# Optimization experiments

Measured on AMD Instinct MI355X. Metric: run time of the kernel, lower is better.

## Reference

```python
import jax, jax.numpy as jnp
import numpy as np

B, H, S, D = 2, 16, 2048, 128

def setup_inputs() -> dict:
    key = jax.random.key(0)
    kq, kk, kv = jax.random.split(key, 3)
    Q = jax.random.normal(kq, (B, H, S, D), dtype=jnp.float32)
    K = jax.random.normal(kk, (B, H, S, D), dtype=jnp.float32)
    V = jax.random.normal(kv, (B, H, S, D), dtype=jnp.float32)
    mask = jnp.tril(jnp.ones((S, S), dtype=bool))  # causal: 1 = keep
    return {"Q": Q, "K": K, "V": V, "mask": mask}

def reference(Q, K, V, mask):
    d_k = Q.shape[-1]
    scale = 1.0 / jnp.sqrt(jnp.asarray(d_k, dtype=Q.dtype))
    # [B,H,S,S] scores, matching the naive materialized implementation's math
    scores = jnp.einsum('bhqd,bhkd->bhqk', Q, K) * scale
    scores = jnp.where(mask, scores, jnp.asarray(-1e9, dtype=scores.dtype))
    attn = jax.nn.softmax(scores, axis=-1)
    return jnp.einsum('bhqk,bhkd->bhqd', attn, V)
```

## Files before the change

kernel.cpp:

```cpp
#include <hip/hip_runtime.h>
#include <hip/hip_bf16.h>
#include <stdint.h>

typedef __attribute__((ext_vector_type(8)))  __bf16 bf16x8;
typedef __attribute__((ext_vector_type(16))) float  f32x16;

#define B_  2
#define H_  16
#define S_  2048
#define D_  128
#define BH_ (B_*H_)

__device__ __forceinline__ uint32_t f2bf1(float f){
  uint32_t u = __builtin_bit_cast(uint32_t, f);
  return (u + 0x7fffu + ((u >> 16) & 1u)) >> 16;
}
__device__ __forceinline__ uint32_t pk2(float a, float b){
  return f2bf1(a) | (f2bf1(b) << 16);
}
__device__ __forceinline__ float bf2f(unsigned short u){
  return __builtin_bit_cast(float, (uint32_t)u << 16);
}
__device__ __forceinline__ float max3f(float a, float b, float c){
  return fmaxf(fmaxf(a, b), c);
}
__device__ __forceinline__ float ex2(float x){
  float r;
  asm("v_exp_f32 %0, %1" : "=v"(r) : "v"(x));
  return r;
}

__device__ __forceinline__ void gld16(const void* g, void* l){
  __builtin_amdgcn_global_load_lds(
      (const __attribute__((address_space(1))) void*)g,
      (__attribute__((address_space(3))) void*)(uintptr_t)l, 16, 0, 0);
}

__device__ const unsigned char SPLIT_TAB[24] = {
  15*4+1,15*4+2, 7*4+0, 14*4+1,14*4+2, 13*4+1,13*4+2, 6*4+0,
  12*4+1,12*4+2, 11*4+1,11*4+2, 5*4+0, 10*4+1,10*4+2, 9*4+1,9*4+2,
  4*4+0, 8*4+1,8*4+2, 3*4+0, 2*4+0, 1*4+0, 0*4+0
};

__global__ void prep(const float* __restrict__ K, const float* __restrict__ V,
                     unsigned short* __restrict__ Kb, unsigned short* __restrict__ Vt){
  __shared__ __attribute__((aligned(16))) unsigned short t[64*68];
  const int kv0 = blockIdx.x * 64, d0 = blockIdx.y * 64, bh = blockIdx.z;
  const int tid = threadIdx.x;
  const float* Vp = V + (size_t)bh * S_ * D_;
  const float* Kp = K + (size_t)bh * S_ * D_;
  unsigned short* Ko = Kb + (size_t)bh * S_ * D_;
  for (int i = 0; i < 4; i++){
    int f = tid + i*256;
    int kv = f >> 4, c4 = f & 15;
    size_t idx = (size_t)(kv0+kv)*D_ + d0 + c4*4;
    float4 k = *(const float4*)(Kp + idx);
    *(uint2*)(Ko + idx) = make_uint2(pk2(k.x,k.y), pk2(k.z,k.w));
  }
  for (int i = 0; i < 4; i++){
    int f = tid + i*256;
    int kv = f >> 4, c4 = f & 15;
    float4 v = *(const float4*)(Vp + (size_t)(kv0+kv)*D_ + d0 + c4*4);
    *(uint2*)&t[kv*68 + c4*4] = make_uint2(pk2(v.x,v.y), pk2(v.z,v.w));
  }
  __syncthreads();
  unsigned short* Vo = Vt + (size_t)bh * D_ * S_;
  for (int i = 0; i < 4; i++){
    int g = tid + i*256;
    int d = g >> 4, c = g & 15, kv = c*4;
    ushort4 o;
    o.x = t[(kv+0)*68 + d];
    o.y = t[(kv+1)*68 + d];
    o.z = t[(kv+2)*68 + d];
    o.w = t[(kv+3)*68 + d];
    *(ushort4*)(Vo + (size_t)(d0+d)*S_ + kv0 + kv) = o;
  }
}

__global__ __launch_bounds__(256, 3)
void attn_fwd(const float* __restrict__ Q, const unsigned short* __restrict__ Kb,
              const unsigned short* __restrict__ Vt, float* __restrict__ Out,
              unsigned short* __restrict__ Opart, float* __restrict__ MLpart,
              int splitFlag){
  __shared__ __attribute__((aligned(16))) unsigned short Klds[2][32*128];
  __shared__ __attribute__((aligned(16))) unsigned short Vlds[2][128*32];

  const int bi = blockIdx.x;
  const int bh = (bi & 7) + 8*((bi >> 3) & 3);
  const int u  = bi >> 5;
  int qb, mode;
  if (splitFlag){ int c = SPLIT_TAB[u]; qb = c >> 2; mode = c & 3; }
  else { qb = (u < 8) ? (15 - u) : (u - 8); mode = 0; }

  const int tid  = threadIdx.x;
  const int wave = tid >> 6, lane = tid & 63;
  const int q32  = lane & 31, hf = lane >> 5;
  const int wq0  = qb*128 + wave*32;
  const int t0   = (mode == 2) ? 2*qb + 2 : 0;
  const int tEnd = (mode == 1) ? 2*qb + 2 : 4*qb + 4;
  const int dtw  = (mode == 1) ? (1 << 30) : (4*qb + wave);
  const float qs = 0.08838834764831845f * 1.44269504088896f;

  const char* Kg = (const char*)(Kb + (size_t)bh * S_ * D_);
  const char* Vg = (const char*)(Vt + (size_t)bh * D_ * S_);

  uint32_t koff[2], voff[2];
  #pragma unroll
  for (int i = 0; i < 2; i++){
    int kr = wave*8 + i*4 + (lane >> 4);
    koff[i] = kr*256 + (((lane & 15) ^ (kr & 15)) << 4);
    int vr = wave*32 + i*16 + (lane >> 2);
    voff[i] = vr*(S_*2) + (((lane & 3) ^ ((vr >> 1) & 3)) << 4);
  }

  auto stage = [&](int buf, int t){
    const char* kp = Kg + t*8192;
    const char* vp = Vg + t*64;
    char* kd = (char*)&Klds[buf][0] + wave*2048;
    char* vd = (char*)&Vlds[buf][0] + wave*2048;
    #pragma unroll
    for (int i = 0; i < 2; i++){
      gld16(kp + koff[i], kd + i*1024);
      gld16(vp + voff[i], vd + i*1024);
    }
  };

  uint4 qf[8];
  {
    const float* Qp = Q + ((size_t)bh * S_ + (wq0 + q32)) * D_ + hf*8;
    #pragma unroll
    for (int ds = 0; ds < 8; ds++){
      float4 a = *(const float4*)(Qp + ds*16);
      float4 b = *(const float4*)(Qp + ds*16 + 4);
      bf16x8 q8;
      q8[0] = (__bf16)(a.x*qs); q8[1] = (__bf16)(a.y*qs);
      q8[2] = (__bf16)(a.z*qs); q8[3] = (__bf16)(a.w*qs);
      q8[4] = (__bf16)(b.x*qs); q8[5] = (__bf16)(b.y*qs);
      q8[6] = (__bf16)(b.z*qs); q8[7] = (__bf16)(b.w*qs);
      qf[ds] = __builtin_bit_cast(uint4, q8);
    }
  }

  f32x16 o[4];
  #pragma unroll
  for (int db = 0; db < 4; db++) o[db] = (f32x16)(0.f);
  float m_run = -INFINITY, l_run = 0.f;

  stage(0, t0);
  __syncthreads();

  int cur = 0;
  for (int t = t0; t < tEnd; ++t){
    if (t + 1 < tEnd) stage(cur ^ 1, t + 1);

    if (t <= dtw){
      const bool diag = (t == dtw);
      const char* Kc = (const char*)&Klds[cur][0];
      const char* Vc = (const char*)&Vlds[cur][0];

      f32x16 sa = (f32x16)(0.f);
      __builtin_amdgcn_s_setprio(1);
      #pragma unroll
      for (int ds = 0; ds < 8; ds++){
        int cb = (q32*256 + ds*32 + hf*16) ^ ((q32 & 15) << 4);
        bf16x8 kf = *(const bf16x8*)(Kc + cb);
        sa = __builtin_amdgcn_mfma_f32_32x32x16_bf16(
               kf, __builtin_bit_cast(bf16x8, qf[ds]), sa, 0, 0, 0);
      }
      __builtin_amdgcn_s_setprio(0);

      float p[16];
      const int q_abs = wq0 + q32;
      #pragma unroll
      for (int r = 0; r < 16; r++){
        float s = sa[r];
        if (diag){
          int kvl = t*32 + (r & 3) + 8*(r >> 2) + 4*hf;
          if (kvl > q_abs) s = -1e30f;
        }
        p[r] = s;
      }
      float a0 = max3f(p[0],  p[1],  p[2]);
      float a1 = max3f(p[3],  p[4],  p[5]);
      float a2 = max3f(p[6],  p[7],  p[8]);
      float a3 = max3f(p[9],  p[10], p[11]);
      float a4 = max3f(p[12], p[13], p[14]);
      float pm = fmaxf(max3f(a0, a1, a2), max3f(a3, a4, p[15]));
      pm = fmaxf(pm, __shfl_xor(pm, 32));
      if (__any(pm > m_run + 11.5f)){
        float mn  = fmaxf(m_run, pm);
        float fac = ex2(m_run - mn);
        float fv[16];
        #pragma unroll
        for (int r = 0; r < 16; r++) fv[r] = __shfl(fac, (r & 3) + 8*(r >> 2) + 4*hf);
        #pragma unroll
        for (int db = 0; db < 4; db++)
          #pragma unroll
          for (int r = 0; r < 16; r++) o[db][r] *= fv[r];
        l_run *= fac;
        m_run = mn;
      }
      float rs = 0.f;
      #pragma unroll
      for (int i = 0; i < 16; i++){ p[i] = ex2(p[i] - m_run); rs += p[i]; }
      rs += __shfl_xor(rs, 32);
      l_run += rs;

      uint32_t Wp[4][2];
      #pragma unroll
      for (int m = 0; m < 4; m++){
        #pragma unroll
        for (int tt = 0; tt < 2; tt++){
          float lo = p[4*m + 2*tt];
          float hi = p[4*m + 2*tt + 1];
          asm("v_cvt_pk_bf16_f32 %0, %1, %2" : "=v"(Wp[m][tt]) : "v"(lo), "v"(hi));
        }
      }

      __builtin_amdgcn_s_setprio(1);
      #pragma unroll
      for (int Ks = 0; Ks < 2; Ks++){
        uint32_t d0 = Wp[2*Ks][0], d2 = Wp[2*Ks + 1][0];
        asm volatile("v_permlane32_swap_b32 %0, %1" : "+v"(d0), "+v"(d2));
        uint32_t d1 = Wp[2*Ks][1], d3 = Wp[2*Ks + 1][1];
        asm volatile("v_permlane32_swap_b32 %0, %1" : "+v"(d1), "+v"(d3));
        uint4 pw = make_uint4(d0, d1, d2, d3);
        bf16x8 paf = __builtin_bit_cast(bf16x8, pw);
        #pragma unroll
        for (int db = 0; db < 4; db++){
          int row = db*32 + q32;
          int vb = (row*64 + Ks*32 + hf*16) ^ (((row >> 1) & 3) << 4);
          bf16x8 vf = *(const bf16x8*)(Vc + vb);
          o[db] = __builtin_amdgcn_mfma_f32_32x32x16_bf16(paf, vf, o[db], 0, 0, 0);
        }
      }
      __builtin_amdgcn_s_setprio(0);
    }

    __syncthreads();
    cur ^= 1;
  }

  if (mode == 0){
    float rl[16];
    #pragma unroll
    for (int r = 0; r < 16; r++)
      rl[r] = 1.f / __shfl(l_run, (r & 3) + 8*(r >> 2) + 4*hf);
    float* Op = Out + ((size_t)bh * S_ + wq0) * D_;
    #pragma unroll
    for (int db = 0; db < 4; db++){
      #pragma unroll
      for (int r = 0; r < 16; r++){
        int qrow = (r & 3) + 8*(r >> 2) + 4*hf;
        Op[(size_t)qrow*D_ + db*32 + q32] = o[db][r] * rl[r];
      }
    }
  } else {
    const int slot = (bh*8 + (qb - 8))*2 + (mode - 1);
    unsigned short* Po = Opart + (size_t)slot * (128*128);
    float* Ml = MLpart + (size_t)slot * 256;
    #pragma unroll
    for (int db = 0; db < 4; db++){
      #pragma unroll
      for (int r = 0; r < 16; r++){
        int row = wave*32 + (r & 3) + 8*(r >> 2) + 4*hf;
        __bf16 bv = (__bf16)o[db][r];
        Po[row*128 + db*32 + q32] = __builtin_bit_cast(unsigned short, bv);
      }
    }
    if (hf == 0){
      Ml[(wave*32 + q32)*2 + 0] = m_run;
      Ml[(wave*32 + q32)*2 + 1] = l_run;
    }
  }
}

__global__ __launch_bounds__(256)
void combine(const unsigned short* __restrict__ Opart,
             const float* __restrict__ MLpart, float* __restrict__ Out){
  const int blk = blockIdx.x;
  const int bh = blk >> 3, qq = blk & 7;
  const unsigned short* A  = Opart + (size_t)(blk*2) * (128*128);
  const unsigned short* Bp = A + 128*128;
  const float* MA = MLpart + (size_t)(blk*2) * 256;
  const float* MB = MA + 256;

  const int row  = threadIdx.x >> 1;
  const int half = threadIdx.x & 1;
  float mA = MA[row*2], lA = MA[row*2 + 1];
  float mB = MB[row*2], lB = MB[row*2 + 1];
  float M  = fmaxf(mA, mB);
  float wA = exp2f(mA - M), wB = exp2f(mB - M);
  float inv = 1.f / (lA*wA + lB*wB);
  wA *= inv; wB *= inv;

  const unsigned short* Ar = A  + row*128 + half*64;
  const unsigned short* Br = Bp + row*128 + half*64;
  float* Or = Out + ((size_t)bh * S_ + (qq + 8)*128 + row) * D_ + half*64;
  #pragma unroll
  for (int c = 0; c < 64; c += 8){
    ushort4 a0 = *(const ushort4*)(Ar + c), a1 = *(const ushort4*)(Ar + c + 4);
    ushort4 b0 = *(const ushort4*)(Br + c), b1 = *(const ushort4*)(Br + c + 4);
    const unsigned short av[8] = {a0.x,a0.y,a0.z,a0.w,a1.x,a1.y,a1.z,a1.w};
    const unsigned short bv[8] = {b0.x,b0.y,b0.z,b0.w,b1.x,b1.y,b1.z,b1.w};
    #pragma unroll
    for (int j = 0; j < 8; j++){
      Or[c + j] = bf2f(av[j])*wA + bf2f(bv[j])*wB;
    }
  }
}

extern "C" void kernel_launch(void* const* d_in, const int* in_sizes, int n_in,
                              void* d_out, int out_size, void* d_ws, size_t ws_size,
                              hipStream_t stream){
  const float* Q = (const float*)d_in[0];
  const float* K = (const float*)d_in[1];
  const float* V = (const float*)d_in[2];
  float* Out = (float*)d_out;

  unsigned short* Kb = (unsigned short*)d_ws;
  unsigned short* Vt = Kb + (size_t)BH_ * S_ * D_;
  unsigned short* Opart = Vt + (size_t)BH_ * S_ * D_;
  float* MLpart = (float*)(Opart + (size_t)512 * 128 * 128);

  const size_t need = (size_t)BH_*S_*D_*2*3 + (size_t)512*256*4;
  const int split = (ws_size >= need) ? 1 : 0;

  prep<<<dim3(S_/64, D_/64, BH_), 256, 0, stream>>>(K, V, Kb, Vt);
  attn_fwd<<<split ? 768 : 512, 256, 0, stream>>>(Q, Kb, Vt, Out, Opart, MLpart, split);
  if (split) combine<<<256, 256, 0, stream>>>(Opart, MLpart, Out);
}
```

Measured before the change: 85.09 us.

## Pre-swizzle K into MFMA fragment layout and load directly from global

The prep kernel now writes bf16 K in a per-tile fragment order that matches the MFMA operand layout, so each lane reads its 16-byte fragment contiguously. The attention kernel drops the K shared-memory double buffer and loads K fragments straight from global/L2 into registers each tile. This removes LDS traffic and staging for K and frees shared memory, but each of the 4 waves now reads the same K tile separately from global memory. That load sits right before the MFMAs with no prefetch, so its latency is exposed.

Result: slower. 90.85 us (+6.8%).

```diff
diff --git a/kernel.cpp b/kernel.cpp
--- a/kernel.cpp
+++ b/kernel.cpp
@@ -43,19 +43,23 @@
 };
 
 __global__ void prep(const float* __restrict__ K, const float* __restrict__ V,
-                     unsigned short* __restrict__ Kb, unsigned short* __restrict__ Vt){
+                     unsigned short* __restrict__ Kf, unsigned short* __restrict__ Vt){
   __shared__ __attribute__((aligned(16))) unsigned short t[64*68];
   const int kv0 = blockIdx.x * 64, d0 = blockIdx.y * 64, bh = blockIdx.z;
   const int tid = threadIdx.x;
   const float* Vp = V + (size_t)bh * S_ * D_;
   const float* Kp = K + (size_t)bh * S_ * D_;
-  unsigned short* Ko = Kb + (size_t)bh * S_ * D_;
+  char* Ko = (char*)(Kf + (size_t)bh * S_ * D_);
   for (int i = 0; i < 4; i++){
     int f = tid + i*256;
     int kv = f >> 4, c4 = f & 15;
-    size_t idx = (size_t)(kv0+kv)*D_ + d0 + c4*4;
-    float4 k = *(const float4*)(Kp + idx);
-    *(uint2*)(Ko + idx) = make_uint2(pk2(k.x,k.y), pk2(k.z,k.w));
+    int kv_g = kv0 + kv;
+    int d = d0 + c4*4;
+    float4 k = *(const float4*)(Kp + (size_t)kv_g*D_ + d);
+    int tt = kv_g >> 5, rr = kv_g & 31;
+    int ds = d >> 4, hi = (d >> 3) & 1, j = d & 7;
+    int byte = tt*8192 + ds*1024 + (rr + 32*hi)*16 + j*2;
+    *(uint2*)(Ko + byte) = make_uint2(pk2(k.x,k.y), pk2(k.z,k.w));
   }
   for (int i = 0; i < 4; i++){
     int f = tid + i*256;
@@ -78,11 +82,10 @@
 }
 
 __global__ __launch_bounds__(256, 3)
-void attn_fwd(const float* __restrict__ Q, const unsigned short* __restrict__ Kb,
+void attn_fwd(const float* __restrict__ Q, const unsigned short* __restrict__ Kf,
               const unsigned short* __restrict__ Vt, float* __restrict__ Out,
               unsigned short* __restrict__ Opart, float* __restrict__ MLpart,
               int splitFlag){
-  __shared__ __attribute__((aligned(16))) unsigned short Klds[2][32*128];
   __shared__ __attribute__((aligned(16))) unsigned short Vlds[2][128*32];
 
   const int bi = blockIdx.x;
@@ -101,26 +104,21 @@
   const int dtw  = (mode == 1) ? (1 << 30) : (4*qb + wave);
   const float qs = 0.08838834764831845f * 1.44269504088896f;
 
-  const char* Kg = (const char*)(Kb + (size_t)bh * S_ * D_);
+  const char* Kg = (const char*)(Kf + (size_t)bh * S_ * D_);
   const char* Vg = (const char*)(Vt + (size_t)bh * D_ * S_);
 
-  uint32_t koff[2], voff[2];
+  uint32_t voff[2];
   #pragma unroll
   for (int i = 0; i < 2; i++){
-    int kr = wave*8 + i*4 + (lane >> 4);
-    koff[i] = kr*256 + (((lane & 15) ^ (kr & 15)) << 4);
     int vr = wave*32 + i*16 + (lane >> 2);
     voff[i] = vr*(S_*2) + (((lane & 3) ^ ((vr >> 1) & 3)) << 4);
   }
 
   auto stage = [&](int buf, int t){
-    const char* kp = Kg + t*8192;
     const char* vp = Vg + t*64;
-    char* kd = (char*)&Klds[buf][0] + wave*2048;
     char* vd = (char*)&Vlds[buf][0] + wave*2048;
     #pragma unroll
     for (int i = 0; i < 2; i++){
-      gld16(kp + koff[i], kd + i*1024);
       gld16(vp + voff[i], vd + i*1024);
     }
   };
@@ -155,17 +153,21 @@
 
     if (t <= dtw){
       const bool diag = (t == dtw);
-      const char* Kc = (const char*)&Klds[cur][0];
       const char* Vc = (const char*)&Vlds[cur][0];
+
+      const char* Kt = Kg + t*8192;
+      uint4 kf[8];
+      #pragma unroll
+      for (int ds = 0; ds < 8; ds++)
+        kf[ds] = *(const uint4*)(Kt + ds*1024 + lane*16);
 
       f32x16 sa = (f32x16)(0.f);
       __builtin_amdgcn_s_setprio(1);
       #pragma unroll
       for (int ds = 0; ds < 8; ds++){
-        int cb = (q32*256 + ds*32 + hf*16) ^ ((q32 & 15) << 4);
-        bf16x8 kf = *(const bf16x8*)(Kc + cb);
         sa = __builtin_amdgcn_mfma_f32_32x32x16_bf16(
-               kf, __builtin_bit_cast(bf16x8, qf[ds]), sa, 0, 0, 0);
+               __builtin_bit_cast(bf16x8, kf[ds]),
+               __builtin_bit_cast(bf16x8, qf[ds]), sa, 0, 0, 0);
       }
       __builtin_amdgcn_s_setprio(0);
 
@@ -318,15 +320,15 @@
   const float* V = (const float*)d_in[2];
   float* Out = (float*)d_out;
 
-  unsigned short* Kb = (unsigned short*)d_ws;
-  unsigned short* Vt = Kb + (size_t)BH_ * S_ * D_;
+  unsigned short* Kf = (unsigned short*)d_ws;
+  unsigned short* Vt = Kf + (size_t)BH_ * S_ * D_;
   unsigned short* Opart = Vt + (size_t)BH_ * S_ * D_;
   float* MLpart = (float*)(Opart + (size_t)512 * 128 * 128);
 
   const size_t need = (size_t)BH_*S_*D_*2*3 + (size_t)512*256*4;
   const int split = (ws_size >= need) ? 1 : 0;
 
-  prep<<<dim3(S_/64, D_/64, BH_), 256, 0, stream>>>(K, V, Kb, Vt);
-  attn_fwd<<<split ? 768 : 512, 256, 0, stream>>>(Q, Kb, Vt, Out, Opart, MLpart, split);
+  prep<<<dim3(S_/64, D_/64, BH_), 256, 0, stream>>>(K, V, Kf, Vt);
+  attn_fwd<<<split ? 768 : 512, 256, 0, stream>>>(Q, Kf, Vt, Out, Opart, MLpart, split);
   if (split) combine<<<256, 256, 0, stream>>>(Opart, MLpart, Out);
 }
```

## Fuse K fp32-to-bf16 conversion into attention kernel's LDS staging

Applied to the files above, without the earlier changes.

Stops converting K to bf16 in the prep kernel. The attention kernel now loads fp32 K tiles into registers early in each iteration, converts them, and writes them to swizzled LDS after the compute step, while V still uses direct global-to-LDS loads. This removes a full pass that writes and re-reads a bf16 K copy in workspace. In exchange, each attention block reads twice as many K bytes (fp32), repeats the conversion for every query block that touches a tile, and holds more registers live across the MFMA loop, which may lower occupancy.

New measurement: 185.1 us. +117.5%, slower.

```diff
diff --git a/kernel.cpp b/kernel.cpp
--- a/kernel.cpp
+++ b/kernel.cpp
@@ -42,21 +42,11 @@
   4*4+0, 8*4+1,8*4+2, 3*4+0, 2*4+0, 1*4+0, 0*4+0
 };
 
-__global__ void prep(const float* __restrict__ K, const float* __restrict__ V,
-                     unsigned short* __restrict__ Kb, unsigned short* __restrict__ Vt){
+__global__ void prep(const float* __restrict__ V, unsigned short* __restrict__ Vt){
   __shared__ __attribute__((aligned(16))) unsigned short t[64*68];
   const int kv0 = blockIdx.x * 64, d0 = blockIdx.y * 64, bh = blockIdx.z;
   const int tid = threadIdx.x;
   const float* Vp = V + (size_t)bh * S_ * D_;
-  const float* Kp = K + (size_t)bh * S_ * D_;
-  unsigned short* Ko = Kb + (size_t)bh * S_ * D_;
-  for (int i = 0; i < 4; i++){
-    int f = tid + i*256;
-    int kv = f >> 4, c4 = f & 15;
-    size_t idx = (size_t)(kv0+kv)*D_ + d0 + c4*4;
-    float4 k = *(const float4*)(Kp + idx);
-    *(uint2*)(Ko + idx) = make_uint2(pk2(k.x,k.y), pk2(k.z,k.w));
-  }
   for (int i = 0; i < 4; i++){
     int f = tid + i*256;
     int kv = f >> 4, c4 = f & 15;
@@ -78,7 +68,7 @@
 }
 
 __global__ __launch_bounds__(256, 3)
-void attn_fwd(const float* __restrict__ Q, const unsigned short* __restrict__ Kb,
+void attn_fwd(const float* __restrict__ Q, const float* __restrict__ Kfp,
               const unsigned short* __restrict__ Vt, float* __restrict__ Out,
               unsigned short* __restrict__ Opart, float* __restrict__ MLpart,
               int splitFlag){
@@ -101,28 +91,42 @@
   const int dtw  = (mode == 1) ? (1 << 30) : (4*qb + wave);
   const float qs = 0.08838834764831845f * 1.44269504088896f;
 
-  const char* Kg = (const char*)(Kb + (size_t)bh * S_ * D_);
-  const char* Vg = (const char*)(Vt + (size_t)bh * D_ * S_);
-
-  uint32_t koff[2], voff[2];
+  const float* Kg = Kfp + (size_t)bh * S_ * D_;
+  const char*  Vg = (const char*)(Vt + (size_t)bh * D_ * S_);
+
+  const int kr  = wave*8 + (lane >> 3);
+  const int c0  = (lane & 7)*16;
+  const float* Kln = Kg + (size_t)kr*D_ + c0;
+  const int kwb = kr*256 + (lane & 7)*32;
+  const int ksz = (kr & 15) << 4;
+
+  uint32_t voff[2];
   #pragma unroll
   for (int i = 0; i < 2; i++){
-    int kr = wave*8 + i*4 + (lane >> 4);
-    koff[i] = kr*256 + (((lane & 15) ^ (kr & 15)) << 4);
     int vr = wave*32 + i*16 + (lane >> 2);
     voff[i] = vr*(S_*2) + (((lane & 3) ^ ((vr >> 1) & 3)) << 4);
   }
 
-  auto stage = [&](int buf, int t){
-    const char* kp = Kg + t*8192;
+  auto stageV = [&](int buf, int t){
     const char* vp = Vg + t*64;
-    char* kd = (char*)&Klds[buf][0] + wave*2048;
     char* vd = (char*)&Vlds[buf][0] + wave*2048;
     #pragma unroll
-    for (int i = 0; i < 2; i++){
-      gld16(kp + koff[i], kd + i*1024);
-      gld16(vp + voff[i], vd + i*1024);
-    }
+    for (int i = 0; i < 2; i++) gld16(vp + voff[i], vd + i*1024);
+  };
+  auto loadK = [&](int t, float4* kq){
+    const float* kp = Kln + (size_t)t*32*D_;
+    #pragma unroll
+    for (int i = 0; i < 4; i++) kq[i] = *(const float4*)(kp + i*4);
+  };
+  auto writeK = [&](int buf, const float4* kq){
+    uint4 w0, w1;
+    w0.x = pk2(kq[0].x, kq[0].y); w0.y = pk2(kq[0].z, kq[0].w);
+    w0.z = pk2(kq[1].x, kq[1].y); w0.w = pk2(kq[1].z, kq[1].w);
+    w1.x = pk2(kq[2].x, kq[2].y); w1.y = pk2(kq[2].z, kq[2].w);
+    w1.z = pk2(kq[3].x, kq[3].y); w1.w = pk2(kq[3].z, kq[3].w);
+    char* base = (char*)&Klds[buf][0];
+    *(uint4*)(base + ( kwb        ^ ksz)) = w0;
+    *(uint4*)(base + ((kwb + 16)  ^ ksz)) = w1;
   };
 
   uint4 qf[8];
@@ -146,12 +150,22 @@
   for (int db = 0; db < 4; db++) o[db] = (f32x16)(0.f);
   float m_run = -INFINITY, l_run = 0.f;
 
-  stage(0, t0);
+  {
+    float4 kq[4];
+    loadK(t0, kq);
+    stageV(0, t0);
+    writeK(0, kq);
+  }
   __syncthreads();
 
+  float4 kq[4];
   int cur = 0;
   for (int t = t0; t < tEnd; ++t){
-    if (t + 1 < tEnd) stage(cur ^ 1, t + 1);
+    const bool pf = (t + 1 < tEnd);
+    if (pf){
+      loadK(t + 1, kq);
+      stageV(cur ^ 1, t + 1);
+    }
 
     if (t <= dtw){
       const bool diag = (t == dtw);
@@ -237,6 +251,7 @@
       __builtin_amdgcn_s_setprio(0);
     }
 
+    if (pf) writeK(cur ^ 1, kq);
     __syncthreads();
     cur ^= 1;
   }
@@ -318,15 +333,14 @@
   const float* V = (const float*)d_in[2];
   float* Out = (float*)d_out;
 
-  unsigned short* Kb = (unsigned short*)d_ws;
-  unsigned short* Vt = Kb + (size_t)BH_ * S_ * D_;
+  unsigned short* Vt = (unsigned short*)d_ws;
   unsigned short* Opart = Vt + (size_t)BH_ * S_ * D_;
   float* MLpart = (float*)(Opart + (size_t)512 * 128 * 128);
 
-  const size_t need = (size_t)BH_*S_*D_*2*3 + (size_t)512*256*4;
+  const size_t need = (size_t)BH_*S_*D_*2*2 + (size_t)512*256*4;
   const int split = (ws_size >= need) ? 1 : 0;
 
-  prep<<<dim3(S_/64, D_/64, BH_), 256, 0, stream>>>(K, V, Kb, Vt);
-  attn_fwd<<<split ? 768 : 512, 256, 0, stream>>>(Q, Kb, Vt, Out, Opart, MLpart, split);
+  prep<<<dim3(S_/64, D_/64, BH_), 256, 0, stream>>>(V, Vt);
+  attn_fwd<<<split ? 768 : 512, 256, 0, stream>>>(Q, K, Vt, Out, Opart, MLpart, split);
   if (split) combine<<<256, 256, 0, stream>>>(Opart, MLpart, Out);
 }
```
